# Performance work log

Hardware: AMD Instinct MI355X
Metric: run time of the kernel (lower is better)

The kernel has to match this reference:

```python
import jax, jax.numpy as jnp
import numpy as np

D_MODEL, D_K, C_DIM = 1024, 64, 64
B, S = 4, 4096


def setup_inputs() -> dict:
    key = jax.random.key(0)
    ks = jax.random.split(key, 10)
    sc = 1.0 / np.sqrt(D_MODEL)
    return {
        "X": jax.random.normal(ks[0], (B, S, D_MODEL), jnp.float32),
        "cultural_embedding": jax.random.normal(ks[1], (B, C_DIM), jnp.float32),
        "WQ": jax.random.normal(ks[2], (D_MODEL, D_K), jnp.float32) * sc,
        "bQ": jnp.zeros((D_K,), jnp.float32),
        "WK": jax.random.normal(ks[3], (D_MODEL, D_K), jnp.float32) * sc,
        "bK": jnp.zeros((D_K,), jnp.float32),
        "WV": jax.random.normal(ks[4], (D_MODEL, D_K), jnp.float32) * sc,
        "bV": jnp.zeros((D_K,), jnp.float32),
        "WC": jax.random.normal(ks[5], (C_DIM, D_K), jnp.float32) * (1.0 / np.sqrt(C_DIM)),
        "bC": jnp.zeros((D_K,), jnp.float32),
        "lam": jnp.float32(1.0),
    }


def reference(X, cultural_embedding, WQ, bQ, WK, bK, WV, bV, WC, bC, lam):
    # Projections: [B,S,d_k]
    Q = jnp.einsum('bsm,mk->bsk', X, WQ) + bQ
    K = jnp.einsum('bsm,mk->bsk', X, WK) + bK
    V = jnp.einsum('bsm,mk->bsk', X, WV) + bV
    # Cultural projection: [B,d_k]
    c_proj = cultural_embedding @ WC + bC
    # Base attention logits [B,S,S]
    base_logits = jnp.einsum('bqk,bsk->bqs', Q, K) / jnp.sqrt(jnp.float32(D_K))
    # Rank-1 cultural bias per query row, scalar lambda gate
    cultural_bias = lam * jnp.einsum('bsd,bd->bs', Q, c_proj)  # [B,S]
    combined = base_logits + cultural_bias[..., None]
    attn = jax.nn.softmax(combined, axis=-1)
    return jnp.einsum('bqs,bsk->bqk', attn, V)
```

## Files before the change

kernel.cpp:

```cpp
#include <hip/hip_runtime.h>

#define B_  4
#define S_  4096
#define DM  1024
#define DK  64
#define NSPLIT 8
#define KSPAN (S_ / NSPLIT)
#define QT  256

typedef _Float16 half8  __attribute__((ext_vector_type(8)));
typedef _Float16 half4v __attribute__((ext_vector_type(4)));
typedef float    floatx4 __attribute__((ext_vector_type(4)));

#define QSCALE 0.18033688011112042f
#define EXP2F(x) __builtin_amdgcn_exp2f(x)

__global__ __launch_bounds__(256) void wt_kernel(
    const float* __restrict__ WQ, const float* __restrict__ WK,
    const float* __restrict__ WV, _Float16* __restrict__ Wt)
{
    const int proj = blockIdx.y;
    const float* W = (proj == 0) ? WQ : (proj == 1) ? WK : WV;
    const int k0 = blockIdx.x * 64;
    const int t = threadIdx.x;
    __shared__ float T[64][68];

    #pragma unroll
    for (int p = 0; p < 4; p++) {
        int c = p * 256 + t;
        int k = c >> 4, n4 = (c & 15) * 4;
        float4 v = *(const float4*)(W + (size_t)(k0 + k) * DK + n4);
        T[k][n4 + 0] = v.x; T[k][n4 + 1] = v.y;
        T[k][n4 + 2] = v.z; T[k][n4 + 3] = v.w;
    }
    __syncthreads();

    const int n = t >> 2, kc = (t & 3) * 16;
    half8 h0, h1;
    #pragma unroll
    for (int j = 0; j < 8; j++) h0[j] = (_Float16)T[kc + j][n];
    #pragma unroll
    for (int j = 0; j < 8; j++) h1[j] = (_Float16)T[kc + 8 + j][n];
    _Float16* dst = Wt + ((size_t)proj * 64 + n) * DM + k0 + kc;
    *(half8*)(dst)     = h0;
    *(half8*)(dst + 8) = h1;
}

__global__ __launch_bounds__(256) void proj_mfma_kernel(
    const float* __restrict__ X, const _Float16* __restrict__ Wt,
    const float* __restrict__ bQ, const float* __restrict__ bK,
    const float* __restrict__ bV,
    _Float16* __restrict__ Qh, _Float16* __restrict__ Kh,
    _Float16* __restrict__ Vt)
{
    const int r0   = blockIdx.x * 64;
    const int t    = threadIdx.x;
    const int wave = t >> 6, lane = t & 63;
    const int quad = lane >> 4, l15 = lane & 15;

    __shared__ __align__(16) _Float16 Xs[64 * 72];
    __shared__ __align__(16) _Float16 Ws[3][64 * 72];

    floatx4 acc[3][4];
    #pragma unroll
    for (int p = 0; p < 3; p++)
        #pragma unroll
        for (int nt = 0; nt < 4; nt++)
            acc[p][nt] = (floatx4){0.f, 0.f, 0.f, 0.f};

    int xrow[4], xcol[4];
    #pragma unroll
    for (int p = 0; p < 4; p++) {
        int c = p * 256 + t;
        xrow[p] = c >> 4; xcol[p] = (c & 15) * 4;
    }
    int wrow[2], wcol[2];
    #pragma unroll
    for (int p = 0; p < 2; p++) {
        int c = p * 256 + t;
        wrow[p] = c >> 3; wcol[p] = (c & 7) * 8;
    }

    float4 xr[4]; half8 wr[3][2];
    #pragma unroll
    for (int p = 0; p < 4; p++)
        xr[p] = *(const float4*)(X + (size_t)(r0 + xrow[p]) * DM + xcol[p]);
    #pragma unroll
    for (int pr = 0; pr < 3; pr++)
        #pragma unroll
        for (int p = 0; p < 2; p++)
            wr[pr][p] = *(const half8*)(Wt + ((size_t)pr * 64 + wrow[p]) * DM + wcol[p]);

    for (int kt = 0; kt < DM / 64; kt++) {
        __syncthreads();
        #pragma unroll
        for (int p = 0; p < 4; p++) {
            half4v h;
            h[0] = (_Float16)xr[p].x; h[1] = (_Float16)xr[p].y;
            h[2] = (_Float16)xr[p].z; h[3] = (_Float16)xr[p].w;
            *(half4v*)&Xs[xrow[p] * 72 + xcol[p]] = h;
        }
        #pragma unroll
        for (int pr = 0; pr < 3; pr++)
            #pragma unroll
            for (int p = 0; p < 2; p++)
                *(half8*)&Ws[pr][wrow[p] * 72 + wcol[p]] = wr[pr][p];
        __syncthreads();

        if (kt + 1 < DM / 64) {
            const int kn = (kt + 1) * 64;
            #pragma unroll
            for (int p = 0; p < 4; p++)
                xr[p] = *(const float4*)(X + (size_t)(r0 + xrow[p]) * DM + kn + xcol[p]);
            #pragma unroll
            for (int pr = 0; pr < 3; pr++)
                #pragma unroll
                for (int p = 0; p < 2; p++)
                    wr[pr][p] = *(const half8*)(Wt + ((size_t)pr * 64 + wrow[p]) * DM + kn + wcol[p]);
        }

        half8 xa0 = *(half8*)&Xs[(wave * 16 + l15) * 72 + quad * 8];
        half8 xa1 = *(half8*)&Xs[(wave * 16 + l15) * 72 + 32 + quad * 8];
        #pragma unroll
        for (int pr = 0; pr < 3; pr++) {
            #pragma unroll
            for (int nt = 0; nt < 4; nt++) {
                half8 bf0 = *(half8*)&Ws[pr][(nt * 16 + l15) * 72 + quad * 8];
                half8 bf1 = *(half8*)&Ws[pr][(nt * 16 + l15) * 72 + 32 + quad * 8];
                floatx4 a = acc[pr][nt];
                a = __builtin_amdgcn_mfma_f32_16x16x32_f16(xa0, bf0, a, 0, 0, 0);
                a = __builtin_amdgcn_mfma_f32_16x16x32_f16(xa1, bf1, a, 0, 0, 0);
                acc[pr][nt] = a;
            }
        }
    }

    float bqv[4], bkv[4], bvv[4];
    #pragma unroll
    for (int nt = 0; nt < 4; nt++) {
        bqv[nt] = bQ[nt * 16 + l15];
        bkv[nt] = bK[nt * 16 + l15];
        bvv[nt] = bV[nt * 16 + l15];
    }

    const int orow = r0 + wave * 16 + quad * 4;
    const int bidx = r0 >> 12;
    const int s0   = (r0 & (S_ - 1)) + wave * 16 + quad * 4;
    #pragma unroll
    for (int nt = 0; nt < 4; nt++) {
        const int d = nt * 16 + l15;
        #pragma unroll
        for (int i = 0; i < 4; i++) {
            Qh[(size_t)(orow + i) * DK + d] =
                (_Float16)((acc[0][nt][i] + bqv[nt]) * QSCALE);
            Kh[(size_t)(orow + i) * DK + d] =
                (_Float16)(acc[1][nt][i] + bkv[nt]);
        }
        half4v hv;
        #pragma unroll
        for (int i = 0; i < 4; i++)
            hv[i] = (_Float16)(acc[2][nt][i] + bvv[nt]);
        *(half4v*)(Vt + (size_t)bidx * DK * S_ + (size_t)d * S_ + s0) = hv;
    }
}

__global__ __launch_bounds__(512, 4) void flash_mfma_kernel(
    const _Float16* __restrict__ Qh, const _Float16* __restrict__ Kh,
    const _Float16* __restrict__ Vt, _Float16* __restrict__ Oph,
    float* __restrict__ Lp)
{
    const int b     = blockIdx.y;
    const int q0    = blockIdx.x * QT;
    const int split = blockIdx.z;
    const int kbase = split * KSPAN;
    const int t     = threadIdx.x;
    const int wave  = t >> 6, lane = t & 63;
    const int quad  = lane >> 4, l15 = lane & 15;

    __shared__ __align__(16) _Float16 Ks[2][64 * 72];
    __shared__ __align__(16) _Float16 Vs[2][64 * 72];
    __shared__ __align__(16) _Float16 Ps[8][16 * 72];

    const _Float16* Qb = Qh + ((size_t)b * S_ + q0) * DK;
    const _Float16* Kb = Kh + ((size_t)b * S_ + kbase) * DK;
    const _Float16* Vb = Vt + (size_t)b * DK * S_ + kbase;

    half8 qf0[2], qf1[2];
    #pragma unroll
    for (int mt = 0; mt < 2; mt++) {
        const _Float16* qr = Qb + (size_t)(wave * 32 + mt * 16 + l15) * DK;
        qf0[mt] = *(const half8*)(qr + quad * 8);
        qf1[mt] = *(const half8*)(qr + 32 + quad * 8);
    }

    _Float16* Pw = &Ps[wave][0];

    floatx4 acc[2][4];
    float rs[2][4];
    #pragma unroll
    for (int mt = 0; mt < 2; mt++) {
        #pragma unroll
        for (int nt = 0; nt < 4; nt++) acc[mt][nt] = (floatx4){0.f,0.f,0.f,0.f};
        #pragma unroll
        for (int i = 0; i < 4; i++) rs[mt][i] = 0.f;
    }

    const int kr = t >> 3, kcol = (t & 7) * 8;
    half8 kreg = *(const half8*)(Kb + (size_t)kr * DK + kcol);
    half8 vreg = *(const half8*)(Vb + (size_t)kr * S_ + kcol);
    *(half8*)&Ks[0][kr * 72 + kcol] = kreg;
    *(half8*)&Vs[0][kr * 72 + kcol] = vreg;

    const int NT = KSPAN / 64;
    int cur = 0;
    for (int it = 0; it < NT; it++) {
        __syncthreads();

        if (it + 1 < NT) {
            const int kn = (it + 1) * 64;
            kreg = *(const half8*)(Kb + (size_t)(kn + kr) * DK + kcol);
            vreg = *(const half8*)(Vb + (size_t)kr * S_ + kn + kcol);
        }

        floatx4 sc[2][4];
        __builtin_amdgcn_s_setprio(1);
        #pragma unroll
        for (int nt = 0; nt < 4; nt++) {
            half8 kf0 = *(half8*)&Ks[cur][(nt * 16 + l15) * 72 + quad * 8];
            half8 kf1 = *(half8*)&Ks[cur][(nt * 16 + l15) * 72 + 32 + quad * 8];
            #pragma unroll
            for (int mt = 0; mt < 2; mt++) {
                floatx4 z = (floatx4){0.f, 0.f, 0.f, 0.f};
                z = __builtin_amdgcn_mfma_f32_16x16x32_f16(qf0[mt], kf0, z, 0, 0, 0);
                z = __builtin_amdgcn_mfma_f32_16x16x32_f16(qf1[mt], kf1, z, 0, 0, 0);
                sc[mt][nt] = z;
            }
        }
        __builtin_amdgcn_s_setprio(0);

        half8 pf0[2], pf1[2];
        #pragma unroll
        for (int mt = 0; mt < 2; mt++) {
            #pragma unroll
            for (int nt = 0; nt < 4; nt++)
                #pragma unroll
                for (int i = 0; i < 4; i++) {
                    float pe = EXP2F(sc[mt][nt][i]);
                    rs[mt][i] += pe;
                    Pw[(quad * 4 + i) * 72 + nt * 16 + l15] = (_Float16)pe;
                }
            pf0[mt] = *(half8*)&Pw[l15 * 72 + quad * 8];
            pf1[mt] = *(half8*)&Pw[l15 * 72 + 32 + quad * 8];
        }

        __builtin_amdgcn_s_setprio(1);
        #pragma unroll
        for (int nt = 0; nt < 4; nt++) {
            half8 vf0 = *(half8*)&Vs[cur][(nt * 16 + l15) * 72 + quad * 8];
            half8 vf1 = *(half8*)&Vs[cur][(nt * 16 + l15) * 72 + 32 + quad * 8];
            #pragma unroll
            for (int mt = 0; mt < 2; mt++) {
                floatx4 a = acc[mt][nt];
                a = __builtin_amdgcn_mfma_f32_16x16x32_f16(pf0[mt], vf0, a, 0, 0, 0);
                a = __builtin_amdgcn_mfma_f32_16x16x32_f16(pf1[mt], vf1, a, 0, 0, 0);
                acc[mt][nt] = a;
            }
        }
        __builtin_amdgcn_s_setprio(0);

        if (it + 1 < NT) {
            *(half8*)&Ks[cur ^ 1][kr * 72 + kcol] = kreg;
            *(half8*)&Vs[cur ^ 1][kr * 72 + kcol] = vreg;
        }
        cur ^= 1;
    }

    const size_t prow = (size_t)split * B_ * S_ + (size_t)b * S_ + q0;
    #pragma unroll
    for (int mt = 0; mt < 2; mt++) {
        float inv[4];
        #pragma unroll
        for (int i = 0; i < 4; i++) {
            float r = rs[mt][i];
            #pragma unroll
            for (int off = 1; off < 16; off <<= 1)
                r += __shfl_xor(r, off, 64);
            rs[mt][i] = r;
            inv[i] = 1.0f / r;
        }
        const int rbase = wave * 32 + mt * 16 + quad * 4;
        #pragma unroll
        for (int nt = 0; nt < 4; nt++)
            #pragma unroll
            for (int i = 0; i < 4; i++)
                Oph[(prow + rbase + i) * DK + nt * 16 + l15] =
                    (_Float16)(acc[mt][nt][i] * inv[i]);
        if (l15 == 0) {
            #pragma unroll
            for (int i = 0; i < 4; i++)
                Lp[prow + rbase + i] = rs[mt][i];
        }
    }
}

__global__ __launch_bounds__(256) void combine_kernel(
    const _Float16* __restrict__ Oph, const float* __restrict__ Lp,
    float* __restrict__ O)
{
    const int r  = blockIdx.x * 16 + (threadIdx.x >> 4);
    const int d4 = (threadIdx.x & 15) * 4;
    const int NR = B_ * S_;

    float lw[NSPLIT], lsum = 0.f;
    #pragma unroll
    for (int s = 0; s < NSPLIT; s++) {
        lw[s] = Lp[(size_t)s * NR + r];
        lsum += lw[s];
    }
    const float inv = 1.0f / lsum;

    float o[4] = {0.f, 0.f, 0.f, 0.f};
    #pragma unroll
    for (int s = 0; s < NSPLIT; s++) {
        half4v h = *(const half4v*)(Oph + ((size_t)s * NR + r) * DK + d4);
        const float w = lw[s];
        #pragma unroll
        for (int j = 0; j < 4; j++) o[j] += w * (float)h[j];
    }
    float4 out;
    out.x = o[0] * inv; out.y = o[1] * inv;
    out.z = o[2] * inv; out.w = o[3] * inv;
    *(float4*)(O + (size_t)r * DK + d4) = out;
}

extern "C" void kernel_launch(void* const* d_in, const int* in_sizes, int n_in,
                              void* d_out, int out_size, void* d_ws, size_t ws_size,
                              hipStream_t stream)
{
    const float* X  = (const float*)d_in[0];
    const float* WQ = (const float*)d_in[2];
    const float* bQ = (const float*)d_in[3];
    const float* WK = (const float*)d_in[4];
    const float* bK = (const float*)d_in[5];
    const float* WV = (const float*)d_in[6];
    const float* bV = (const float*)d_in[7];

    char* ws = (char*)d_ws;
    _Float16* Qh  = (_Float16*)ws;  ws += (size_t)B_ * S_ * DK * 2;
    _Float16* Kh  = (_Float16*)ws;  ws += (size_t)B_ * S_ * DK * 2;
    _Float16* Vt  = (_Float16*)ws;  ws += (size_t)B_ * S_ * DK * 2;
    _Float16* Wt  = (_Float16*)ws;  ws += (size_t)3 * 64 * DM * 2;
    _Float16* Oph = (_Float16*)ws;  ws += (size_t)NSPLIT * B_ * S_ * DK * 2;
    float* Lp     = (float*)ws;

    wt_kernel<<<dim3(DM / 64, 3), 256, 0, stream>>>(WQ, WK, WV, Wt);

    proj_mfma_kernel<<<dim3((B_ * S_) / 64), 256, 0, stream>>>(
        X, Wt, bQ, bK, bV, Qh, Kh, Vt);

    flash_mfma_kernel<<<dim3(S_ / QT, B_, NSPLIT), 512, 0, stream>>>(
        Qh, Kh, Vt, Oph, Lp);

    combine_kernel<<<dim3((B_ * S_) / 16), 256, 0, stream>>>(
        Oph, Lp, (float*)d_out);
}
```

Baseline: 155.0 us.

## Keep softmax probabilities in registers by transposing MFMA operands and permuting K rows

```diff
diff --git a/kernel.cpp b/kernel.cpp
--- a/kernel.cpp
+++ b/kernel.cpp
@@ -10,6 +10,7 @@
 
 typedef _Float16 half8  __attribute__((ext_vector_type(8)));
 typedef _Float16 half4v __attribute__((ext_vector_type(4)));
+typedef __fp16   fp16x2 __attribute__((ext_vector_type(2)));
 typedef float    floatx4 __attribute__((ext_vector_type(4)));
 
 #define QSCALE 0.18033688011112042f
@@ -179,7 +180,6 @@
 
     __shared__ __align__(16) _Float16 Ks[2][64 * 72];
     __shared__ __align__(16) _Float16 Vs[2][64 * 72];
-    __shared__ __align__(16) _Float16 Ps[8][16 * 72];
 
     const _Float16* Qb = Qh + ((size_t)b * S_ + q0) * DK;
     const _Float16* Kb = Kh + ((size_t)b * S_ + kbase) * DK;
@@ -193,23 +193,21 @@
         qf1[mt] = *(const half8*)(qr + 32 + quad * 8);
     }
 
-    _Float16* Pw = &Ps[wave][0];
-
     floatx4 acc[2][4];
-    float rs[2][4];
+    float rs[2];
     #pragma unroll
     for (int mt = 0; mt < 2; mt++) {
         #pragma unroll
         for (int nt = 0; nt < 4; nt++) acc[mt][nt] = (floatx4){0.f,0.f,0.f,0.f};
-        #pragma unroll
-        for (int i = 0; i < 4; i++) rs[mt][i] = 0.f;
-    }
-
-    const int kr = t >> 3, kcol = (t & 7) * 8;
+        rs[mt] = 0.f;
+    }
+
+    const int kr   = t >> 3, kcol = (t & 7) * 8;
+    const int krP  = (kr & 32) | ((kr & 4) << 2) | ((kr & 24) >> 1) | (kr & 3);
     half8 kreg = *(const half8*)(Kb + (size_t)kr * DK + kcol);
     half8 vreg = *(const half8*)(Vb + (size_t)kr * S_ + kcol);
-    *(half8*)&Ks[0][kr * 72 + kcol] = kreg;
-    *(half8*)&Vs[0][kr * 72 + kcol] = vreg;
+    *(half8*)&Ks[0][krP * 72 + kcol] = kreg;
+    *(half8*)&Vs[0][kr  * 72 + kcol] = vreg;
 
     const int NT = KSPAN / 64;
     int cur = 0;
@@ -231,8 +229,8 @@
             #pragma unroll
             for (int mt = 0; mt < 2; mt++) {
                 floatx4 z = (floatx4){0.f, 0.f, 0.f, 0.f};
-                z = __builtin_amdgcn_mfma_f32_16x16x32_f16(qf0[mt], kf0, z, 0, 0, 0);
-                z = __builtin_amdgcn_mfma_f32_16x16x32_f16(qf1[mt], kf1, z, 0, 0, 0);
+                z = __builtin_amdgcn_mfma_f32_16x16x32_f16(kf0, qf0[mt], z, 0, 0, 0);
+                z = __builtin_amdgcn_mfma_f32_16x16x32_f16(kf1, qf1[mt], z, 0, 0, 0);
                 sc[mt][nt] = z;
             }
         }
@@ -241,16 +239,30 @@
         half8 pf0[2], pf1[2];
         #pragma unroll
         for (int mt = 0; mt < 2; mt++) {
+            float pe[4][4];
             #pragma unroll
             for (int nt = 0; nt < 4; nt++)
                 #pragma unroll
                 for (int i = 0; i < 4; i++) {
-                    float pe = EXP2F(sc[mt][nt][i]);
-                    rs[mt][i] += pe;
-                    Pw[(quad * 4 + i) * 72 + nt * 16 + l15] = (_Float16)pe;
+                    pe[nt][i] = EXP2F(sc[mt][nt][i]);
+                    rs[mt] += pe[nt][i];
                 }
-            pf0[mt] = *(half8*)&Pw[l15 * 72 + quad * 8];
-            pf1[mt] = *(half8*)&Pw[l15 * 72 + 32 + quad * 8];
+            fp16x2 c0 = __builtin_amdgcn_cvt_pkrtz(pe[0][0], pe[0][1]);
+            fp16x2 c1 = __builtin_amdgcn_cvt_pkrtz(pe[0][2], pe[0][3]);
+            fp16x2 c2 = __builtin_amdgcn_cvt_pkrtz(pe[1][0], pe[1][1]);
+            fp16x2 c3 = __builtin_amdgcn_cvt_pkrtz(pe[1][2], pe[1][3]);
+            pf0[mt] = (half8){(_Float16)c0[0], (_Float16)c0[1],
+                              (_Float16)c1[0], (_Float16)c1[1],
+                              (_Float16)c2[0], (_Float16)c2[1],
+                              (_Float16)c3[0], (_Float16)c3[1]};
+            fp16x2 c4 = __builtin_amdgcn_cvt_pkrtz(pe[2][0], pe[2][1]);
+            fp16x2 c5 = __builtin_amdgcn_cvt_pkrtz(pe[2][2], pe[2][3]);
+            fp16x2 c6 = __builtin_amdgcn_cvt_pkrtz(pe[3][0], pe[3][1]);
+            fp16x2 c7 = __builtin_amdgcn_cvt_pkrtz(pe[3][2], pe[3][3]);
+            pf1[mt] = (half8){(_Float16)c4[0], (_Float16)c4[1],
+                              (_Float16)c5[0], (_Float16)c5[1],
+                              (_Float16)c6[0], (_Float16)c6[1],
+                              (_Float16)c7[0], (_Float16)c7[1]};
         }
 
         __builtin_amdgcn_s_setprio(1);
@@ -261,16 +273,16 @@
             #pragma unroll
             for (int mt = 0; mt < 2; mt++) {
                 floatx4 a = acc[mt][nt];
-                a = __builtin_amdgcn_mfma_f32_16x16x32_f16(pf0[mt], vf0, a, 0, 0, 0);
-                a = __builtin_amdgcn_mfma_f32_16x16x32_f16(pf1[mt], vf1, a, 0, 0, 0);
+                a = __builtin_amdgcn_mfma_f32_16x16x32_f16(vf0, pf0[mt], a, 0, 0, 0);
+                a = __builtin_amdgcn_mfma_f32_16x16x32_f16(vf1, pf1[mt], a, 0, 0, 0);
                 acc[mt][nt] = a;
             }
         }
         __builtin_amdgcn_s_setprio(0);
 
         if (it + 1 < NT) {
-            *(half8*)&Ks[cur ^ 1][kr * 72 + kcol] = kreg;
-            *(half8*)&Vs[cur ^ 1][kr * 72 + kcol] = vreg;
+            *(half8*)&Ks[cur ^ 1][krP * 72 + kcol] = kreg;
+            *(half8*)&Vs[cur ^ 1][kr  * 72 + kcol] = vreg;
         }
         cur ^= 1;
     }
@@ -278,28 +290,21 @@
     const size_t prow = (size_t)split * B_ * S_ + (size_t)b * S_ + q0;
     #pragma unroll
     for (int mt = 0; mt < 2; mt++) {
-        float inv[4];
-        #pragma unroll
-        for (int i = 0; i < 4; i++) {
-            float r = rs[mt][i];
-            #pragma unroll
-            for (int off = 1; off < 16; off <<= 1)
-                r += __shfl_xor(r, off, 64);
-            rs[mt][i] = r;
-            inv[i] = 1.0f / r;
-        }
-        const int rbase = wave * 32 + mt * 16 + quad * 4;
-        #pragma unroll
-        for (int nt = 0; nt < 4; nt++)
+        float r = rs[mt];
+        r += __shfl_xor(r, 16, 64);
+        r += __shfl_xor(r, 32, 64);
+        const float inv = 1.0f / r;
+        const size_t orow = prow + wave * 32 + mt * 16 + l15;
+        #pragma unroll
+        for (int nt = 0; nt < 4; nt++) {
+            half4v hv;
             #pragma unroll
             for (int i = 0; i < 4; i++)
-                Oph[(prow + rbase + i) * DK + nt * 16 + l15] =
-                    (_Float16)(acc[mt][nt][i] * inv[i]);
-        if (l15 == 0) {
-            #pragma unroll
-            for (int i = 0; i < 4; i++)
-                Lp[prow + rbase + i] = rs[mt][i];
-        }
+                hv[i] = (_Float16)(acc[mt][nt][i] * inv);
+            *(half4v*)(Oph + orow * DK + nt * 16 + quad * 4) = hv;
+        }
+        if (quad == 0)
+            Lp[orow] = r;
     }
 }
 
```

After: 151.8 us. -2.1%, faster.
